# Optimization experiments

Hardware: AMD Instinct MI355X
Metric: run time of the kernel (lower is better)

## Reference

```python
import jax, jax.numpy as jnp
import numpy as np

N_LEVELS = 16
N_FEATS = 2
LOG2_HASH = 19
HASH_SIZE = 1 << LOG2_HASH
BASE_RES = 16
FINEST_RES = 512
_b = np.exp((np.log(FINEST_RES) - np.log(BASE_RES)) / (N_LEVELS - 1))
RESOLUTIONS = [int(np.ceil(BASE_RES * _b ** i)) for i in range(N_LEVELS)]
PRIMES = jnp.array([1, 2654435761, 805459861], dtype=jnp.uint32)
# all 8 corner offsets of a voxel, ordered (i,j,k) like the torch triple loop
OFFSETS = jnp.array([[i, j, k] for i in range(2) for j in range(2) for k in range(2)], dtype=jnp.int32)  # (8,3)


def _hash(corners):
    # corners: (..., 3) int32. Matches torch int64 (c0*p0 ^ c1*p1 ^ c2*p2) % 2^19:
    # XOR and mod-2^19 depend only on low bits, so uint32 arithmetic is exact.
    c = corners.astype(jnp.uint32) * PRIMES  # (...,3)
    h = c[..., 0] ^ c[..., 1] ^ c[..., 2]
    return (h & jnp.uint32(HASH_SIZE - 1)).astype(jnp.int32)


def setup_inputs() -> dict:
    key = jax.random.key(0)
    kx, kt = jax.random.split(key)
    x = jax.random.uniform(kx, (2097152, 3), dtype=jnp.float32)
    tables = jax.random.normal(kt, (N_LEVELS, HASH_SIZE, N_FEATS), dtype=jnp.float32) * 0.01
    return {"x": x, "tables": tables}


def reference(x, tables):
    x = jnp.clip(x, 0.0, 1.0 - 1e-6)  # (N,3)
    outs = []
    for level, res in enumerate(RESOLUTIONS):
        scaled = x * res                                # (N,3)
        floor = jnp.floor(scaled)
        w = scaled - floor                              # (N,3) trilinear frac
        floor_i = floor.astype(jnp.int32)
        corners = floor_i[:, None, :] + OFFSETS[None, :, :]   # (N,8,3)
        idx = _hash(corners)                            # (N,8)
        feats = tables[level][idx]                      # (N,8,F) hash gather
        # per-corner trilinear weight: prod over dims of (w if offset else 1-w)
        cw = jnp.where(OFFSETS[None, :, :] == 1, w[:, None, :], 1.0 - w[:, None, :])  # (N,8,3)
        cw = cw[:, :, 0] * cw[:, :, 1] * cw[:, :, 2]    # (N,8)
        outs.append(jnp.einsum('nc,ncf->nf', cw, feats))  # (N,F)
    return jnp.concatenate(outs, axis=-1)               # (N, L*F)
```

## Files before the change

kernel.cpp:

```cpp
#include <hip/hip_runtime.h>
#include <math.h>

#define NL 16
#define HASH_SIZE (1u << 19)
#define HASH_MASK (HASH_SIZE - 1u)
#define P1 2654435761u
#define P2 805459861u
#define PTS_PER_BLOCK 1024
#define THREADS 256
#define BX 32
#define NB (BX * BX * BX)
#define SCAN_BLOCKS (NB / THREADS)

typedef float f2 __attribute__((ext_vector_type(2)));
typedef float f4 __attribute__((ext_vector_type(4)));

struct Res16 { float r[NL]; };

__device__ __forceinline__ void clamp3(float& px, float& py, float& pz)
{
    px = fminf(fmaxf(px, 0.0f), 0.999999f);
    py = fminf(fmaxf(py, 0.0f), 0.999999f);
    pz = fminf(fmaxf(pz, 0.0f), 0.999999f);
}

__device__ __forceinline__ f2 enc_pl_simple(const f2* __restrict__ tb, float r,
                                            float px, float py, float pz)
{
    float sx = px * r, sy = py * r, sz = pz * r;
    float fx = floorf(sx), fy = floorf(sy), fz = floorf(sz);
    float wx = sx - fx, wy = sy - fy, wz = sz - fz;
    unsigned ix = (unsigned)(int)fx;
    unsigned iy = (unsigned)(int)fy;
    unsigned iz = (unsigned)(int)fz;
    unsigned hx0 = ix,      hx1 = ix + 1u;
    unsigned hy0 = iy * P1, hy1 = hy0 + P1;
    unsigned hz0 = iz * P2, hz1 = hz0 + P2;

    f2 f000 = tb[(hx0 ^ hy0 ^ hz0) & HASH_MASK];
    f2 f001 = tb[(hx0 ^ hy0 ^ hz1) & HASH_MASK];
    f2 f010 = tb[(hx0 ^ hy1 ^ hz0) & HASH_MASK];
    f2 f011 = tb[(hx0 ^ hy1 ^ hz1) & HASH_MASK];
    f2 f100 = tb[(hx1 ^ hy0 ^ hz0) & HASH_MASK];
    f2 f101 = tb[(hx1 ^ hy0 ^ hz1) & HASH_MASK];
    f2 f110 = tb[(hx1 ^ hy1 ^ hz0) & HASH_MASK];
    f2 f111 = tb[(hx1 ^ hy1 ^ hz1) & HASH_MASK];

    float wx0 = 1.0f - wx, wy0 = 1.0f - wy, wz0 = 1.0f - wz;
    float c000 = (wx0 * wy0) * wz0, c001 = (wx0 * wy0) * wz;
    float c010 = (wx0 * wy ) * wz0, c011 = (wx0 * wy ) * wz;
    float c100 = (wx  * wy0) * wz0, c101 = (wx  * wy0) * wz;
    float c110 = (wx  * wy ) * wz0, c111 = (wx  * wy ) * wz;

    float a0 = c000 * f000.x + c001 * f001.x + c010 * f010.x + c011 * f011.x
             + c100 * f100.x + c101 * f101.x + c110 * f110.x + c111 * f111.x;
    float a1 = c000 * f000.y + c001 * f001.y + c010 * f010.y + c011 * f011.y
             + c100 * f100.y + c101 * f101.y + c110 * f110.y + c111 * f111.y;
    f2 ret; ret.x = a0; ret.y = a1;
    return ret;
}

__device__ __forceinline__ f2 enc_pl_merged(const f2* __restrict__ tb, float r,
                                            float px, float py, float pz)
{
    float sx = px * r, sy = py * r, sz = pz * r;
    float fx = floorf(sx), fy = floorf(sy), fz = floorf(sz);
    float wx = sx - fx, wy = sy - fy, wz = sz - fz;
    unsigned ix = (unsigned)(int)fx;
    unsigned iy = (unsigned)(int)fy;
    unsigned iz = (unsigned)(int)fz;
    unsigned hy0 = iy * P1, hy1 = hy0 + P1;
    unsigned hz0 = iz * P2, hz1 = hz0 + P2;
    f2 f000, f001, f010, f011, f100, f101, f110, f111;
    if ((ix & 1u) == 0u) {
        const f4* __restrict__ tb4 = reinterpret_cast<const f4*>(tb);
        unsigned g00 = (ix ^ hy0 ^ hz0) & HASH_MASK;
        unsigned g01 = (ix ^ hy0 ^ hz1) & HASH_MASK;
        unsigned g10 = (ix ^ hy1 ^ hz0) & HASH_MASK;
        unsigned g11 = (ix ^ hy1 ^ hz1) & HASH_MASK;
        f4 v00 = tb4[g00 >> 1]; f4 v01 = tb4[g01 >> 1];
        f4 v10 = tb4[g10 >> 1]; f4 v11 = tb4[g11 >> 1];
        f2 lo, hi;
        lo.x = v00.x; lo.y = v00.y; hi.x = v00.z; hi.y = v00.w;
        f000 = (g00 & 1u) ? hi : lo;  f100 = (g00 & 1u) ? lo : hi;
        lo.x = v01.x; lo.y = v01.y; hi.x = v01.z; hi.y = v01.w;
        f001 = (g01 & 1u) ? hi : lo;  f101 = (g01 & 1u) ? lo : hi;
        lo.x = v10.x; lo.y = v10.y; hi.x = v10.z; hi.y = v10.w;
        f010 = (g10 & 1u) ? hi : lo;  f110 = (g10 & 1u) ? lo : hi;
        lo.x = v11.x; lo.y = v11.y; hi.x = v11.z; hi.y = v11.w;
        f011 = (g11 & 1u) ? hi : lo;  f111 = (g11 & 1u) ? lo : hi;
    } else {
        unsigned hx0 = ix, hx1 = ix + 1u;
        f000 = tb[(hx0 ^ hy0 ^ hz0) & HASH_MASK];
        f001 = tb[(hx0 ^ hy0 ^ hz1) & HASH_MASK];
        f010 = tb[(hx0 ^ hy1 ^ hz0) & HASH_MASK];
        f011 = tb[(hx0 ^ hy1 ^ hz1) & HASH_MASK];
        f100 = tb[(hx1 ^ hy0 ^ hz0) & HASH_MASK];
        f101 = tb[(hx1 ^ hy0 ^ hz1) & HASH_MASK];
        f110 = tb[(hx1 ^ hy1 ^ hz0) & HASH_MASK];
        f111 = tb[(hx1 ^ hy1 ^ hz1) & HASH_MASK];
    }
    float wx0 = 1.0f - wx, wy0 = 1.0f - wy, wz0 = 1.0f - wz;
    float c000 = (wx0 * wy0) * wz0, c001 = (wx0 * wy0) * wz;
    float c010 = (wx0 * wy ) * wz0, c011 = (wx0 * wy ) * wz;
    float c100 = (wx  * wy0) * wz0, c101 = (wx  * wy0) * wz;
    float c110 = (wx  * wy ) * wz0, c111 = (wx  * wy ) * wz;
    float a0 = c000 * f000.x + c001 * f001.x + c010 * f010.x + c011 * f011.x
             + c100 * f100.x + c101 * f101.x + c110 * f110.x + c111 * f111.x;
    float a1 = c000 * f000.y + c001 * f001.y + c010 * f010.y + c011 * f011.y
             + c100 * f100.y + c101 * f101.y + c110 * f110.y + c111 * f111.y;
    f2 ret; ret.x = a0; ret.y = a1;
    return ret;
}

__global__ __launch_bounds__(THREADS) void hist_kernel(
    const float* __restrict__ x, int* __restrict__ hist, int N)
{
    __shared__ int lh[NB];
    for (int i = threadIdx.x; i < NB; i += THREADS) lh[i] = 0;
    __syncthreads();
    for (int n = blockIdx.x * THREADS + threadIdx.x; n < N;
         n += gridDim.x * THREADS) {
        float px = x[3 * (size_t)n + 0];
        float py = x[3 * (size_t)n + 1];
        float pz = x[3 * (size_t)n + 2];
        clamp3(px, py, pz);
        int bin = ((int)(pz * BX) * BX + (int)(py * BX)) * BX + (int)(px * BX);
        atomicAdd(&lh[bin], 1);
    }
    __syncthreads();
    for (int i = threadIdx.x; i < NB; i += THREADS)
        if (lh[i]) atomicAdd(&hist[i], lh[i]);
}

__global__ __launch_bounds__(THREADS) void scan1_kernel(
    const int* __restrict__ hist, int* __restrict__ bsum)
{
    __shared__ int sm[THREADS];
    int t = threadIdx.x;
    sm[t] = hist[blockIdx.x * THREADS + t];
    __syncthreads();
    for (int off = THREADS / 2; off > 0; off >>= 1) {
        if (t < off) sm[t] += sm[t + off];
        __syncthreads();
    }
    if (t == 0) bsum[blockIdx.x] = sm[0];
}

__global__ __launch_bounds__(SCAN_BLOCKS) void scan2_kernel(
    const int* __restrict__ bsum, int* __restrict__ bpre)
{
    __shared__ int sm[SCAN_BLOCKS];
    int t = threadIdx.x;
    int v = bsum[t];
    sm[t] = v;
    __syncthreads();
    for (int off = 1; off < SCAN_BLOCKS; off <<= 1) {
        int u = (t >= off) ? sm[t - off] : 0;
        __syncthreads();
        sm[t] += u;
        __syncthreads();
    }
    bpre[t] = sm[t] - v;
}

__global__ __launch_bounds__(THREADS) void scan3_kernel(
    const int* __restrict__ hist, const int* __restrict__ bpre,
    int* __restrict__ cursor)
{
    __shared__ int sm[THREADS];
    int t = threadIdx.x;
    int v = hist[blockIdx.x * THREADS + t];
    sm[t] = v;
    __syncthreads();
    for (int off = 1; off < THREADS; off <<= 1) {
        int u = (t >= off) ? sm[t - off] : 0;
        __syncthreads();
        sm[t] += u;
        __syncthreads();
    }
    cursor[blockIdx.x * THREADS + t] = bpre[blockIdx.x] + sm[t] - v;
}

__global__ __launch_bounds__(THREADS) void scatter_kernel(
    const float* __restrict__ x, int* __restrict__ cursor,
    float* __restrict__ sx, int* __restrict__ perm, int N)
{
    int n = blockIdx.x * THREADS + threadIdx.x;
    if (n >= N) return;
    float px = x[3 * (size_t)n + 0];
    float py = x[3 * (size_t)n + 1];
    float pz = x[3 * (size_t)n + 2];
    clamp3(px, py, pz);
    int bin = ((int)(pz * BX) * BX + (int)(py * BX)) * BX + (int)(px * BX);
    int pos = atomicAdd(&cursor[bin], 1);
    f4 v; v.x = px; v.y = py; v.z = pz; v.w = 0.0f;
    *reinterpret_cast<f4*>(sx + (size_t)pos * 4) = v;
    perm[pos] = n;
}

__global__ __launch_bounds__(THREADS) void hashenc_coarse_kernel(
    const float* __restrict__ sx, const float* __restrict__ tables,
    float* __restrict__ ws, int N, int nchunks, Res16 res)
{
    int level = blockIdx.x & 7;
    int chunk = blockIdx.x >> 3;
    float r = res.r[level];
    const f2* __restrict__ tb =
        reinterpret_cast<const f2*>(tables) + (size_t)level * HASH_SIZE;
    f2* __restrict__ wl = reinterpret_cast<f2*>(ws) + (size_t)level * N;
    int base = chunk * PTS_PER_BLOCK + threadIdx.x;
#pragma unroll
    for (int i = 0; i < PTS_PER_BLOCK / THREADS; ++i) {
        int n = base + i * THREADS;
        if (n >= N) break;
        f4 p = __builtin_nontemporal_load(
            reinterpret_cast<const f4*>(sx + (size_t)n * 4));
        f2 a = enc_pl_simple(tb, r, p.x, p.y, p.z);
        __builtin_nontemporal_store(a, wl + n);
    }
}

__global__ __launch_bounds__(THREADS) void hashenc_fine_kernel(
    const float* __restrict__ sx, const float* __restrict__ tb_f,
    float* __restrict__ wl_f, int N, float r)
{
    const f2* __restrict__ tb = reinterpret_cast<const f2*>(tb_f);
    f2* __restrict__ wl = reinterpret_cast<f2*>(wl_f);
    int base = blockIdx.x * PTS_PER_BLOCK + threadIdx.x;
#pragma unroll
    for (int i = 0; i < PTS_PER_BLOCK / THREADS; ++i) {
        int n = base + i * THREADS;
        if (n >= N) break;
        f4 p = __builtin_nontemporal_load(
            reinterpret_cast<const f4*>(sx + (size_t)n * 4));
        f2 a = enc_pl_merged(tb, r, p.x, p.y, p.z);
        __builtin_nontemporal_store(a, wl + n);
    }
}

__global__ __launch_bounds__(THREADS) void hashenc_transpose_kernel(
    const float* __restrict__ ws, const int* __restrict__ perm,
    float* __restrict__ out, int N)
{
    int c    = threadIdx.x & 7;
    int pid  = threadIdx.x >> 3;
    int base = blockIdx.x * 256;
    const f2* __restrict__ w2 = reinterpret_cast<const f2*>(ws);
#pragma unroll
    for (int i = 0; i < 8; ++i) {
        int p = base + i * 32 + pid;
        if (p >= N) return;
        f2 a = __builtin_nontemporal_load(w2 + (size_t)(2 * c)     * N + p);
        f2 b = __builtin_nontemporal_load(w2 + (size_t)(2 * c + 1) * N + p);
        int o = perm[p];
        f4 v; v.x = a.x; v.y = a.y; v.z = b.x; v.w = b.y;
        __builtin_nontemporal_store(
            v, reinterpret_cast<f4*>(out + (size_t)o * (2 * NL) + c * 4));
    }
}

__global__ __launch_bounds__(THREADS) void hashenc_level_nosort_kernel(
    const float* __restrict__ x, const float* __restrict__ tables,
    float* __restrict__ ws, int N, int nchunks, Res16 res)
{
    int slot  = blockIdx.x & 7;
    int rest  = blockIdx.x >> 3;
    int chunk = rest % nchunks;
    int phase = rest / nchunks;
    int level = phase * 8 + slot;
    float r = res.r[level];
    const f2* __restrict__ tb =
        reinterpret_cast<const f2*>(tables) + (size_t)level * HASH_SIZE;
    f2* __restrict__ wl = reinterpret_cast<f2*>(ws) + (size_t)level * N;
    int base = chunk * PTS_PER_BLOCK + threadIdx.x;
#pragma unroll
    for (int i = 0; i < PTS_PER_BLOCK / THREADS; ++i) {
        int n = base + i * THREADS;
        if (n >= N) break;
        float px = __builtin_nontemporal_load(x + 3 * (size_t)n + 0);
        float py = __builtin_nontemporal_load(x + 3 * (size_t)n + 1);
        float pz = __builtin_nontemporal_load(x + 3 * (size_t)n + 2);
        clamp3(px, py, pz);
        f2 a = enc_pl_merged(tb, r, px, py, pz);
        __builtin_nontemporal_store(a, wl + n);
    }
}

__global__ __launch_bounds__(THREADS) void hashenc_transpose_nosort_kernel(
    const float* __restrict__ ws, float* __restrict__ out, int N)
{
    int c    = threadIdx.x & 7;
    int pid  = threadIdx.x >> 3;
    int base = blockIdx.x * 256;
    const f2* __restrict__ w2 = reinterpret_cast<const f2*>(ws);
#pragma unroll
    for (int i = 0; i < 8; ++i) {
        int p = base + i * 32 + pid;
        if (p >= N) return;
        f2 a = __builtin_nontemporal_load(w2 + (size_t)(2 * c)     * N + p);
        f2 b = __builtin_nontemporal_load(w2 + (size_t)(2 * c + 1) * N + p);
        f4 v; v.x = a.x; v.y = a.y; v.z = b.x; v.w = b.y;
        __builtin_nontemporal_store(
            v, reinterpret_cast<f4*>(out + (size_t)p * (2 * NL) + c * 4));
    }
}

__global__ __launch_bounds__(THREADS) void hashenc_mono_kernel(
    const float* __restrict__ x, const float* __restrict__ tables,
    float* __restrict__ out, int N, Res16 res)
{
    int n = blockIdx.x * THREADS + threadIdx.x;
    if (n >= N) return;
    float px = x[3 * (size_t)n + 0], py = x[3 * (size_t)n + 1], pz = x[3 * (size_t)n + 2];
    clamp3(px, py, pz);
    float acc[2 * NL];
#pragma unroll
    for (int l = 0; l < NL; ++l) {
        const f2* tb = reinterpret_cast<const f2*>(tables) + (size_t)l * HASH_SIZE;
        f2 a = enc_pl_merged(tb, res.r[l], px, py, pz);
        acc[2 * l] = a.x; acc[2 * l + 1] = a.y;
    }
    f4* o = reinterpret_cast<f4*>(out + (size_t)n * (2 * NL));
#pragma unroll
    for (int q = 0; q < 8; ++q) {
        f4 v; v.x = acc[4*q]; v.y = acc[4*q+1]; v.z = acc[4*q+2]; v.w = acc[4*q+3];
        o[q] = v;
    }
}

extern "C" void kernel_launch(void* const* d_in, const int* in_sizes, int n_in,
                              void* d_out, int out_size, void* d_ws, size_t ws_size,
                              hipStream_t stream)
{
    const float* x      = (const float*)d_in[0];
    const float* tables = (const float*)d_in[1];
    float* out          = (float*)d_out;
    int N = in_sizes[0] / 3;

    Res16 res;
    double b = exp((log(512.0) - log(16.0)) / 15.0);
    for (int i = 0; i < NL; ++i)
        res.r[i] = (float)(int)ceil(16.0 * pow(b, (double)i));

    size_t enc_f      = (size_t)NL * N * 2;
    size_t need_sort  = (enc_f + (size_t)N * 5 + 2 * NB + 2 * SCAN_BLOCKS) * sizeof(float);
    size_t need_plain = enc_f * sizeof(float);

    if (ws_size >= need_sort) {
        float* wse    = (float*)d_ws;
        float* sx     = wse + enc_f;
        int*   perm   = (int*)(sx + (size_t)N * 4);
        int*   hist   = perm + N;
        int*   cursor = hist + NB;
        int*   bsum   = cursor + NB;
        int*   bpre   = bsum + SCAN_BLOCKS;

        hipMemsetAsync(hist, 0, NB * sizeof(int), stream);
        hipLaunchKernelGGL(hist_kernel, dim3(256), dim3(THREADS), 0, stream,
                           x, hist, N);
        hipLaunchKernelGGL(scan1_kernel, dim3(SCAN_BLOCKS), dim3(THREADS), 0, stream,
                           hist, bsum);
        hipLaunchKernelGGL(scan2_kernel, dim3(1), dim3(SCAN_BLOCKS), 0, stream,
                           bsum, bpre);
        hipLaunchKernelGGL(scan3_kernel, dim3(SCAN_BLOCKS), dim3(THREADS), 0, stream,
                           hist, bpre, cursor);
        hipLaunchKernelGGL(scatter_kernel, dim3((N + THREADS - 1) / THREADS),
                           dim3(THREADS), 0, stream, x, cursor, sx, perm, N);

        int nchunks = (N + PTS_PER_BLOCK - 1) / PTS_PER_BLOCK;
        hipLaunchKernelGGL(hashenc_coarse_kernel, dim3(8 * nchunks),
                           dim3(THREADS), 0, stream, sx, tables, wse, N, nchunks, res);
        for (int l = 8; l < NL; ++l) {
            hipLaunchKernelGGL(hashenc_fine_kernel, dim3(nchunks), dim3(THREADS),
                               0, stream,
                               sx,
                               (const float*)(tables + (size_t)l * HASH_SIZE * 2),
                               wse + (size_t)l * N * 2,
                               N, res.r[l]);
        }
        hipLaunchKernelGGL(hashenc_transpose_kernel, dim3((N + 255) / 256),
                           dim3(THREADS), 0, stream, wse, perm, out, N);
    } else if (ws_size >= need_plain) {
        int nchunks = (N + PTS_PER_BLOCK - 1) / PTS_PER_BLOCK;
        hipLaunchKernelGGL(hashenc_level_nosort_kernel, dim3(2 * 8 * nchunks),
                           dim3(THREADS), 0, stream, x, tables, (float*)d_ws,
                           N, nchunks, res);
        hipLaunchKernelGGL(hashenc_transpose_nosort_kernel, dim3((N + 255) / 256),
                           dim3(THREADS), 0, stream, (const float*)d_ws, out, N);
    } else {
        hipLaunchKernelGGL(hashenc_mono_kernel, dim3((N + THREADS - 1) / THREADS),
                           dim3(THREADS), 0, stream, x, tables, out, N, res);
    }
}
```

Before: 825.9 us.

## Fuse coarse-level encoding into the transpose kernel and halve the workspace

Drops the separate coarse-level kernel. Each of the 8 lanes per point in the transpose kernel now computes one coarse level (0-7), and warp shuffles regroup the results so the lanes that own levels 0-7 write them straight to the output. The remaining lanes read the fine levels from the workspace, which now holds only 8 levels. This removes the workspace write and reread for the coarse levels and one launch. In exchange, coarse gathers happen inside the transpose, where the 8 lanes of a point hit 8 different tables, and nontemporal hints are dropped from the fine kernel while being added to the x loads.

```diff
diff --git a/kernel.cpp b/kernel.cpp
--- a/kernel.cpp
+++ b/kernel.cpp
@@ -2,6 +2,7 @@
 #include <math.h>
 
 #define NL 16
+#define NFINE 8
 #define HASH_SIZE (1u << 19)
 #define HASH_MASK (HASH_SIZE - 1u)
 #define P1 2654435761u
@@ -121,9 +122,9 @@
     __syncthreads();
     for (int n = blockIdx.x * THREADS + threadIdx.x; n < N;
          n += gridDim.x * THREADS) {
-        float px = x[3 * (size_t)n + 0];
-        float py = x[3 * (size_t)n + 1];
-        float pz = x[3 * (size_t)n + 2];
+        float px = __builtin_nontemporal_load(x + 3 * (size_t)n + 0);
+        float py = __builtin_nontemporal_load(x + 3 * (size_t)n + 1);
+        float pz = __builtin_nontemporal_load(x + 3 * (size_t)n + 2);
         clamp3(px, py, pz);
         int bin = ((int)(pz * BX) * BX + (int)(py * BX)) * BX + (int)(px * BX);
         atomicAdd(&lh[bin], 1);
@@ -188,9 +189,9 @@
 {
     int n = blockIdx.x * THREADS + threadIdx.x;
     if (n >= N) return;
-    float px = x[3 * (size_t)n + 0];
-    float py = x[3 * (size_t)n + 1];
-    float pz = x[3 * (size_t)n + 2];
+    float px = __builtin_nontemporal_load(x + 3 * (size_t)n + 0);
+    float py = __builtin_nontemporal_load(x + 3 * (size_t)n + 1);
+    float pz = __builtin_nontemporal_load(x + 3 * (size_t)n + 2);
     clamp3(px, py, pz);
     int bin = ((int)(pz * BX) * BX + (int)(py * BX)) * BX + (int)(px * BX);
     int pos = atomicAdd(&cursor[bin], 1);
@@ -199,64 +200,63 @@
     perm[pos] = n;
 }
 
-__global__ __launch_bounds__(THREADS) void hashenc_coarse_kernel(
-    const float* __restrict__ sx, const float* __restrict__ tables,
-    float* __restrict__ ws, int N, int nchunks, Res16 res)
-{
-    int level = blockIdx.x & 7;
-    int chunk = blockIdx.x >> 3;
-    float r = res.r[level];
-    const f2* __restrict__ tb =
-        reinterpret_cast<const f2*>(tables) + (size_t)level * HASH_SIZE;
-    f2* __restrict__ wl = reinterpret_cast<f2*>(ws) + (size_t)level * N;
-    int base = chunk * PTS_PER_BLOCK + threadIdx.x;
+__global__ __launch_bounds__(THREADS) void hashenc_fine_kernel(
+    const float* __restrict__ sx, const float* __restrict__ tb_f,
+    float* __restrict__ wl_f, int N, float r)
+{
+    const f2* __restrict__ tb = reinterpret_cast<const f2*>(tb_f);
+    f2* __restrict__ wl = reinterpret_cast<f2*>(wl_f);
+    int base = blockIdx.x * PTS_PER_BLOCK + threadIdx.x;
 #pragma unroll
     for (int i = 0; i < PTS_PER_BLOCK / THREADS; ++i) {
         int n = base + i * THREADS;
         if (n >= N) break;
-        f4 p = __builtin_nontemporal_load(
-            reinterpret_cast<const f4*>(sx + (size_t)n * 4));
-        f2 a = enc_pl_simple(tb, r, p.x, p.y, p.z);
-        __builtin_nontemporal_store(a, wl + n);
-    }
-}
-
-__global__ __launch_bounds__(THREADS) void hashenc_fine_kernel(
-    const float* __restrict__ sx, const float* __restrict__ tb_f,
-    float* __restrict__ wl_f, int N, float r)
-{
-    const f2* __restrict__ tb = reinterpret_cast<const f2*>(tb_f);
-    f2* __restrict__ wl = reinterpret_cast<f2*>(wl_f);
-    int base = blockIdx.x * PTS_PER_BLOCK + threadIdx.x;
-#pragma unroll
-    for (int i = 0; i < PTS_PER_BLOCK / THREADS; ++i) {
-        int n = base + i * THREADS;
-        if (n >= N) break;
-        f4 p = __builtin_nontemporal_load(
-            reinterpret_cast<const f4*>(sx + (size_t)n * 4));
+        f4 p = *reinterpret_cast<const f4*>(sx + (size_t)n * 4);
         f2 a = enc_pl_merged(tb, r, p.x, p.y, p.z);
-        __builtin_nontemporal_store(a, wl + n);
-    }
-}
-
-__global__ __launch_bounds__(THREADS) void hashenc_transpose_kernel(
-    const float* __restrict__ ws, const int* __restrict__ perm,
-    float* __restrict__ out, int N)
+        wl[n] = a;
+    }
+}
+
+__global__ __launch_bounds__(THREADS) void hashenc_transpose_fused_kernel(
+    const float* __restrict__ ws,
+    const float* __restrict__ sx,
+    const int* __restrict__ perm,
+    const float* __restrict__ tables,
+    float* __restrict__ out, int N, Res16 res)
 {
     int c    = threadIdx.x & 7;
     int pid  = threadIdx.x >> 3;
+    int lane = threadIdx.x & 63;
     int base = blockIdx.x * 256;
     const f2* __restrict__ w2 = reinterpret_cast<const f2*>(ws);
+    const f2* __restrict__ tbc =
+        reinterpret_cast<const f2*>(tables) + (size_t)c * HASH_SIZE;
+    float rc = res.r[c];
+    int srcA = (lane & ~7) | ((2 * c) & 7);
+    int srcB = srcA + 1;
 #pragma unroll
     for (int i = 0; i < 8; ++i) {
-        int p = base + i * 32 + pid;
-        if (p >= N) return;
-        f2 a = __builtin_nontemporal_load(w2 + (size_t)(2 * c)     * N + p);
-        f2 b = __builtin_nontemporal_load(w2 + (size_t)(2 * c + 1) * N + p);
-        int o = perm[p];
-        f4 v; v.x = a.x; v.y = a.y; v.z = b.x; v.w = b.y;
-        __builtin_nontemporal_store(
-            v, reinterpret_cast<f4*>(out + (size_t)o * (2 * NL) + c * 4));
+        int p  = base + i * 32 + pid;
+        int pc = p < N ? p : N - 1;
+        f4 pt = *reinterpret_cast<const f4*>(sx + (size_t)pc * 4);
+        f2 mine = enc_pl_simple(tbc, rc, pt.x, pt.y, pt.z);
+        float Ax = __shfl(mine.x, srcA, 64);
+        float Ay = __shfl(mine.y, srcA, 64);
+        float Bx = __shfl(mine.x, srcB, 64);
+        float By = __shfl(mine.y, srcB, 64);
+        f4 v;
+        if (c < 4) {
+            v.x = Ax; v.y = Ay; v.z = Bx; v.w = By;
+        } else {
+            f2 a = w2[(size_t)(2 * c - 8) * N + pc];
+            f2 b = w2[(size_t)(2 * c - 7) * N + pc];
+            v.x = a.x; v.y = a.y; v.z = b.x; v.w = b.y;
+        }
+        if (p < N) {
+            int o = perm[p];
+            __builtin_nontemporal_store(
+                v, reinterpret_cast<f4*>(out + (size_t)o * (2 * NL) + c * 4));
+        }
     }
 }
 
@@ -343,9 +343,9 @@
     for (int i = 0; i < NL; ++i)
         res.r[i] = (float)(int)ceil(16.0 * pow(b, (double)i));
 
-    size_t enc_f      = (size_t)NL * N * 2;
+    size_t enc_f      = (size_t)NFINE * N * 2;
     size_t need_sort  = (enc_f + (size_t)N * 5 + 2 * NB + 2 * SCAN_BLOCKS) * sizeof(float);
-    size_t need_plain = enc_f * sizeof(float);
+    size_t need_plain = (size_t)NL * N * 2 * sizeof(float);
 
     if (ws_size >= need_sort) {
         float* wse    = (float*)d_ws;
@@ -369,18 +369,17 @@
                            dim3(THREADS), 0, stream, x, cursor, sx, perm, N);
 
         int nchunks = (N + PTS_PER_BLOCK - 1) / PTS_PER_BLOCK;
-        hipLaunchKernelGGL(hashenc_coarse_kernel, dim3(8 * nchunks),
-                           dim3(THREADS), 0, stream, sx, tables, wse, N, nchunks, res);
         for (int l = 8; l < NL; ++l) {
             hipLaunchKernelGGL(hashenc_fine_kernel, dim3(nchunks), dim3(THREADS),
                                0, stream,
                                sx,
                                (const float*)(tables + (size_t)l * HASH_SIZE * 2),
-                               wse + (size_t)l * N * 2,
+                               wse + (size_t)(l - 8) * N * 2,
                                N, res.r[l]);
         }
-        hipLaunchKernelGGL(hashenc_transpose_kernel, dim3((N + 255) / 256),
-                           dim3(THREADS), 0, stream, wse, perm, out, N);
+        hipLaunchKernelGGL(hashenc_transpose_fused_kernel, dim3((N + 255) / 256),
+                           dim3(THREADS), 0, stream, wse, sx, perm, tables, out,
+                           N, res);
     } else if (ws_size >= need_plain) {
         int nchunks = (N + PTS_PER_BLOCK - 1) / PTS_PER_BLOCK;
         hipLaunchKernelGGL(hashenc_level_nosort_kernel, dim3(2 * 8 * nchunks),
```

New measurement: 671.0 us. 18.8% less time.
